# Optimization experiments

Measured on AMD Instinct MI355X. Metric: run time of the kernel, lower is better.

Reference implementation:

```python
import jax, jax.numpy as jnp
import numpy as np

B, L, LC, C, CTX, H = 4, 2048, 512, 1024, 1024, 16
D = C // H
EPS = 1e-6
SCALE = 1.0 / np.float32(np.sqrt(D))


def _ln(x):
    # LayerNorm32, elementwise_affine applied outside when present
    mu = jnp.mean(x, axis=-1, keepdims=True)
    var = jnp.var(x, axis=-1, keepdims=True)
    return (x - mu) * jax.lax.rsqrt(var + EPS)


def _attn(q, k, v):
    # q: [B,Lq,H,D], k/v: [B,Lk,H,D] -> [B,Lq,C]
    s = jnp.einsum('bqhd,bkhd->bhqk', q, k) * SCALE
    p = jax.nn.softmax(s, axis=-1)
    o = jnp.einsum('bhqk,bkhd->bqhd', p, v)
    return o.reshape(o.shape[0], o.shape[1], C)


def setup_inputs() -> dict:
    key = jax.random.key(0)
    ks = jax.random.split(key, 12)
    s = 0.02
    w = lambda k, shape: (jax.random.normal(k, shape, jnp.float32) * s)
    z = lambda n: jnp.zeros((n,), jnp.float32)
    return {
        'x': jax.random.normal(ks[0], (B, L, C), jnp.float32),
        'mod': jax.random.normal(ks[1], (B, C), jnp.float32),
        'context': jax.random.normal(ks[2], (B, LC, CTX), jnp.float32),
        'w_ada': w(ks[3], (C, 6 * C)), 'b_ada': z(6 * C),
        'w_qkv': w(ks[4], (C, 3 * C)), 'b_qkv': z(3 * C),
        'w_so': w(ks[5], (C, C)), 'b_so': z(C),
        'g_n2': jnp.ones((C,), jnp.float32), 'b_n2': z(C),
        'w_cq': w(ks[6], (C, C)), 'b_cq': z(C),
        'w_ckv': w(ks[7], (CTX, 2 * C)), 'b_ckv': z(2 * C),
        'w_co': w(ks[8], (C, C)), 'b_co': z(C),
        'w_m1': w(ks[9], (C, 4 * C)), 'b_m1': z(4 * C),
        'w_m2': w(ks[10], (4 * C, C)), 'b_m2': z(C),
    }


def reference(x, mod, context, w_ada, b_ada, w_qkv, b_qkv, w_so, b_so,
              g_n2, b_n2, w_cq, b_cq, w_ckv, b_ckv, w_co, b_co,
              w_m1, b_m1, w_m2, b_m2):
    # adaLN modulation: SiLU -> Linear(C, 6C) -> chunk(6)
    ada = jax.nn.silu(mod) @ w_ada + b_ada  # [B, 6C]
    sh_msa, sc_msa, g_msa, sh_mlp, sc_mlp, g_mlp = jnp.split(ada, 6, axis=-1)
    ex = lambda t: t[:, None, :]  # broadcast per-sample over its token run

    # --- MSA branch ---
    h = _ln(x) * (1.0 + ex(sc_msa)) + ex(sh_msa)
    qkv = (h @ w_qkv + b_qkv).reshape(B, L, 3, H, D)
    h = _attn(qkv[:, :, 0], qkv[:, :, 1], qkv[:, :, 2]) @ w_so + b_so
    x = x + h * ex(g_msa)

    # --- MCA branch (norm2 has affine) ---
    h = _ln(x) * g_n2 + b_n2
    q = (h @ w_cq + b_cq).reshape(B, L, H, D)
    kv = (context @ w_ckv + b_ckv).reshape(B, LC, 2, H, D)
    h = _attn(q, kv[:, :, 0], kv[:, :, 1]) @ w_co + b_co
    x = x + h

    # --- FFN branch ---
    h = _ln(x) * (1.0 + ex(sc_mlp)) + ex(sh_mlp)
    h = jax.nn.gelu(h @ w_m1 + b_m1, approximate=False) @ w_m2 + b_m2
    x = x + h * ex(g_mlp)
    return x
```

## Files before the change

### kernel.cpp

```cpp
#include <hip/hip_runtime.h>
#include <cstdint>

typedef __bf16 bf16;
typedef __bf16 bf16x8 __attribute__((ext_vector_type(8)));
typedef __bf16 bf16x4 __attribute__((ext_vector_type(4)));
typedef float  floatx4 __attribute__((ext_vector_type(4)));
typedef unsigned int uint32x4 __attribute__((ext_vector_type(4)));

#define B_  4
#define L_  2048
#define LC_ 512
#define C_  1024
#define H_  16
#define D_  64

typedef const __attribute__((address_space(1))) unsigned int* as1_u32p;
typedef __attribute__((address_space(3))) unsigned int* as3_u32p;

__device__ __forceinline__ void async16(const void* g, void* l) {
  __builtin_amdgcn_global_load_lds((as1_u32p)g, (as3_u32p)l, 16, 0, 0);
}

__device__ __forceinline__ floatx4 mfma16(bf16x8 a, bf16x8 b, floatx4 c) {
  return __builtin_amdgcn_mfma_f32_16x16x32_bf16(a, b, c, 0, 0, 0);
}

__device__ __forceinline__ bool dt_bf16(const unsigned* dt) { return dt[0] == 0x3F803F80u; }

__device__ __forceinline__ float rd(const void* p, size_t i, bool bf) {
  return bf ? (float)((const bf16*)p)[i] : ((const float*)p)[i];
}

__global__ __launch_bounds__(256) void k_cvt(const void* __restrict__ src, bf16* __restrict__ dst,
                                             int N, const unsigned* __restrict__ dt) {
  bool bf = dt_bf16(dt);
  int i = (blockIdx.x * 256 + threadIdx.x) * 4;
  if (i + 3 < N) {
    for (int j = 0; j < 4; ++j) dst[i + j] = (bf16)rd(src, i + j, bf);
  } else {
    for (int j = 0; j < 4 && i + j < N; ++j) dst[i + j] = (bf16)rd(src, i + j, bf);
  }
}

struct CvtSrcs { const void* s[9]; };
__global__ __launch_bounds__(256) void k_cvt_all(CvtSrcs c, bf16* __restrict__ dst,
                                                 const unsigned* __restrict__ dt) {
  bool bf = dt_bf16(dt);
  int i = blockIdx.x * 256 + threadIdx.x;
  if (i >= 15360) return;
  const int pre[10] = {0, 3072, 4096, 5120, 6144, 7168, 9216, 10240, 14336, 15360};
  int seg = 0;
  #pragma unroll
  for (int k = 1; k < 9; ++k) if (i >= pre[k]) seg = k;
  dst[i] = (bf16)rd(c.s[seg], i - pre[seg], bf);
}

__global__ __launch_bounds__(256) void k_silu(const void* __restrict__ mod, float* __restrict__ sm,
                                              const unsigned* __restrict__ dt) {
  bool bf = dt_bf16(dt);
  int i = blockIdx.x * 256 + threadIdx.x;
  if (i < B_ * C_) {
    float v = rd(mod, i, bf);
    sm[i] = v / (1.f + __expf(-v));
  }
}

__global__ __launch_bounds__(256) void k_ada(const float* __restrict__ sm, const void* __restrict__ w,
                                             float* __restrict__ part, const unsigned* __restrict__ dt) {
  bool bf = dt_bf16(dt);
  int idx = blockIdx.x * 256 + threadIdx.x;
  int b = idx / 6144, j = idx - b * 6144;
  int k0 = blockIdx.y * 256;
  const float* s = sm + b * C_;
  float acc = 0.f;
  if (bf) {
    const bf16* W = (const bf16*)w;
    for (int k = k0; k < k0 + 256; ++k) acc += s[k] * (float)W[(size_t)k * 6144 + j];
  } else {
    const float* W = (const float*)w;
    for (int k = k0; k < k0 + 256; ++k) acc += s[k] * W[(size_t)k * 6144 + j];
  }
  part[(size_t)blockIdx.y * 24576 + idx] = acc;
}

__global__ __launch_bounds__(256) void k_ada_red(const float* __restrict__ part, const void* __restrict__ bv,
                                                 float* __restrict__ ada, const unsigned* __restrict__ dt) {
  bool bf = dt_bf16(dt);
  int idx = blockIdx.x * 256 + threadIdx.x;
  int j = idx % 6144;
  ada[idx] = rd(bv, j, bf) + part[idx] + part[24576 + idx] + part[49152 + idx] + part[73728 + idx];
}

struct TransDesc { const void* src; bf16* dst; int R, Cc, nCb, pre; };
struct TransDescs { TransDesc d[7]; };
__global__ __launch_bounds__(256) void k_trans_all(TransDescs t, const unsigned* __restrict__ dt) {
  bool bf = dt_bf16(dt);
  __shared__ bf16 tile[32][33];
  int blk = blockIdx.x;
  int di = 0;
  #pragma unroll
  for (int i = 1; i < 7; ++i) if (blk >= t.d[i].pre) di = i;
  const void* src = t.d[di].src;
  bf16* dst = t.d[di].dst;
  int R = t.d[di].R, Cc = t.d[di].Cc;
  int local = blk - t.d[di].pre;
  int bx = local % t.d[di].nCb, by = local / t.d[di].nCb;
  int c0 = bx * 32, r0 = by * 32;
  int tx = threadIdx.x & 31, ty = threadIdx.x >> 5;
  for (int i = 0; i < 4; ++i)
    tile[ty * 4 + i][tx] = (bf16)rd(src, (size_t)(r0 + ty * 4 + i) * Cc + c0 + tx, bf);
  __syncthreads();
  for (int i = 0; i < 4; ++i)
    dst[(size_t)(c0 + ty * 4 + i) * R + r0 + tx] = tile[tx][ty * 4 + i];
}

__global__ __launch_bounds__(256) void k_vt(const bf16* __restrict__ src, int ld, int off, int Lk,
                                            bf16* __restrict__ VT) {
  __shared__ bf16 tile[32][33];
  int l0 = blockIdx.x * 32;
  int d0 = blockIdx.y * 32;
  int bh = blockIdx.z, b = bh >> 4, h = bh & 15;
  int tx = threadIdx.x & 31, ty = threadIdx.x >> 5;
  for (int i = 0; i < 4; ++i) {
    int l = l0 + ty * 4 + i;
    tile[ty * 4 + i][tx] = src[((size_t)b * Lk + l) * ld + off + h * 64 + d0 + tx];
  }
  __syncthreads();
  for (int i = 0; i < 4; ++i) {
    int d = d0 + ty * 4 + i;
    VT[((size_t)bh * 64 + d) * Lk + l0 + tx] = tile[tx][ty * 4 + i];
  }
}

__global__ __launch_bounds__(256) void k_ln(const void* __restrict__ xraw, const float* __restrict__ xf,
                                            const unsigned* __restrict__ dt, bf16* __restrict__ out,
                                            const float* __restrict__ ada, int scOff, int shOff, float scAdd,
                                            const bf16* __restrict__ gcol, const bf16* __restrict__ bcol) {
  int row = blockIdx.x;
  int b = row >> 11;
  int base = row * C_ + threadIdx.x * 4;
  float v[4];
  if (xf) {
    for (int i = 0; i < 4; ++i) v[i] = xf[base + i];
  } else {
    bool bf = dt_bf16(dt);
    for (int i = 0; i < 4; ++i) v[i] = rd(xraw, base + i, bf);
  }
  float s1 = 0.f, s2 = 0.f;
  for (int i = 0; i < 4; ++i) { s1 += v[i]; s2 += v[i] * v[i]; }
  for (int m = 1; m < 64; m <<= 1) { s1 += __shfl_xor(s1, m); s2 += __shfl_xor(s2, m); }
  __shared__ float r1[4], r2[4];
  int w = threadIdx.x >> 6;
  if ((threadIdx.x & 63) == 0) { r1[w] = s1; r2[w] = s2; }
  __syncthreads();
  s1 = r1[0] + r1[1] + r1[2] + r1[3];
  s2 = r2[0] + r2[1] + r2[2] + r2[3];
  float mu = s1 * (1.f / (float)C_);
  float var = fmaxf(s2 * (1.f / (float)C_) - mu * mu, 0.f);
  float rstd = rsqrtf(var + 1e-6f);
  for (int i = 0; i < 4; ++i) {
    int c = threadIdx.x * 4 + i;
    float sc, sh;
    if (ada) { sc = scAdd + ada[b * 6144 + scOff + c]; sh = ada[b * 6144 + shOff + c]; }
    else     { sc = (float)gcol[c];                    sh = (float)bcol[c]; }
    out[base + i] = (bf16)((v[i] - mu) * rstd * sc + sh);
  }
}

template <int MODE>
__global__ __launch_bounds__(256) void k_gemm(const bf16* __restrict__ A, const bf16* __restrict__ Bt,
                                              const bf16* __restrict__ bias, void* __restrict__ outv,
                                              int M, int N, int K,
                                              const void* __restrict__ resid,
                                              const float* __restrict__ ada, int gateOff,
                                              const unsigned* __restrict__ dt,
                                              float qs, int qN) {
  __shared__ bf16 As[2 * 128 * 32];
  __shared__ bf16 Bs[2 * 128 * 32];
  const int tid = threadIdx.x;
  const int w = tid >> 6, lane = tid & 63;
  const int wr = w & 1, wc = w >> 1;
  const int g = lane >> 4, t = lane & 15;

  const int nbx = gridDim.x;
  const int nwg = nbx * gridDim.y;
  const int orig = blockIdx.y * nbx + blockIdx.x;
  const int qq = nwg >> 3, rrm = nwg & 7;
  const int xcd = orig & 7, sidx = orig >> 3;
  const int wgid = (xcd < rrm ? xcd * (qq + 1) : rrm * (qq + 1) + (xcd - rrm) * qq) + sidx;
  const int rowA0 = (wgid / nbx) * 128, rowB0 = (wgid % nbx) * 128;

  const bf16* Ag = A  + (size_t)(rowA0 + w * 32 + (lane >> 2)) * K + (lane & 3) * 8;
  const bf16* Bg = Bt + (size_t)(rowB0 + w * 32 + (lane >> 2)) * K + (lane & 3) * 8;
  bf16* As0 = As + w * 1024;
  bf16* Bs0 = Bs + w * 1024;

  floatx4 acc[4][4];
  for (int i = 0; i < 4; ++i) for (int j = 0; j < 4; ++j) for (int r = 0; r < 4; ++r) acc[i][j][r] = 0.f;

  for (int kb = 0; kb < K; kb += 64) {
    async16(Ag + kb,                      As0);
    async16(Ag + kb + (size_t)16 * K,     As0 + 512);
    async16(Ag + kb + 32,                 As0 + 4096);
    async16(Ag + kb + 32 + (size_t)16 * K, As0 + 4096 + 512);
    async16(Bg + kb,                      Bs0);
    async16(Bg + kb + (size_t)16 * K,     Bs0 + 512);
    async16(Bg + kb + 32,                 Bs0 + 4096);
    async16(Bg + kb + 32 + (size_t)16 * K, Bs0 + 4096 + 512);
    __syncthreads();
    #pragma unroll
    for (int kk = 0; kk < 2; ++kk) {
      bf16x8 af[4], bfr[4];
      #pragma unroll
      for (int mt = 0; mt < 4; ++mt) af[mt]  = *(const bf16x8*)&As[kk * 4096 + (wr * 64 + mt * 16 + t) * 32 + g * 8];
      #pragma unroll
      for (int nt = 0; nt < 4; ++nt) bfr[nt] = *(const bf16x8*)&Bs[kk * 4096 + (wc * 64 + nt * 16 + t) * 32 + g * 8];
      #pragma unroll
      for (int mt = 0; mt < 4; ++mt)
        #pragma unroll
        for (int nt = 0; nt < 4; ++nt)
          acc[mt][nt] = mfma16(af[mt], bfr[nt], acc[mt][nt]);
    }
    __syncthreads();
  }

  const bool bf = (MODE == 1 || MODE == 4) ? dt_bf16(dt) : false;
  for (int mt = 0; mt < 4; ++mt) {
    for (int nt = 0; nt < 4; ++nt) {
      int grow = rowA0 + wr * 64 + mt * 16 + g * 4;
      int gcol = rowB0 + wc * 64 + nt * 16 + t;
      float bvv = (float)bias[gcol];
      for (int r = 0; r < 4; ++r) {
        int rr = grow + r;
        float v = acc[mt][nt][r] + bvv;
        size_t idx = (size_t)rr * N + gcol;
        if (MODE == 0) {
          ((bf16*)outv)[idx] = (bf16)(v * ((gcol < qN) ? qs : 1.0f));
        } else if (MODE == 1) {
          float gt = ada[(rr >> 11) * 6144 + gateOff + gcol];
          ((float*)outv)[idx] = rd(resid, idx, bf) + v * gt;
        } else if (MODE == 2) {
          ((float*)outv)[idx] = ((const float*)resid)[idx] + v;
        } else if (MODE == 3) {
          ((bf16*)outv)[idx] = (bf16)(0.5f * v * (1.f + erff(v * 0.70710678118654752f)));
        } else {
          float gt = ada[(rr >> 11) * 6144 + gateOff + gcol];
          float val = ((const float*)resid)[idx] + v * gt;
          if (bf) ((bf16*)outv)[idx] = (bf16)val;
          else    ((float*)outv)[idx] = val;
        }
      }
    }
  }
}

__global__ __launch_bounds__(256) void k_attn(const bf16* __restrict__ Qb, int ldq, int qoff,
                                              const bf16* __restrict__ Kb, int ldk, int koff,
                                              const bf16* __restrict__ VT,
                                              bf16* __restrict__ Ob, int Lk) {
  __shared__ bf16 smem[20480];

  const int tid = threadIdx.x;
  const int w = tid >> 6, lane = tid & 63;
  const int g = lane >> 4, t = lane & 15;
  const int bh = blockIdx.y, b = bh >> 4, h = bh & 15;
  const int q0 = blockIdx.x * 64;

  const bf16* Q  = Qb + (size_t)(b * L_ + q0) * ldq + h * 64 + qoff;
  const bf16* K  = Kb + (size_t)b * Lk * ldk + h * 64 + koff;
  const bf16* Vt = VT + (size_t)bh * 64 * Lk;
  bf16* O = Ob + ((size_t)(b * L_ + q0 + w * 16 + t)) * C_ + h * 64;

  const int sr0 = w * 16 + (lane >> 3), sp = lane & 7;
  const int sr1 = sr0 + 8;
  const int sw0 = (sp ^ (sr0 & 7)) * 8;
  const int sw1 = (sp ^ (sr1 & 7)) * 8;

  bf16* Ps  = smem;
  bf16* KB0 = smem + 4096;
  bf16* VB0 = smem + 12288;

  async16(Q + (size_t)sr0 * ldq + sw0, smem + w * 1024);
  async16(Q + (size_t)sr1 * ldq + sw1, smem + w * 1024 + 512);
  async16(K + (size_t)sr0 * ldk + sw0, KB0 + w * 1024);
  async16(K + (size_t)sr1 * ldk + sw1, KB0 + w * 1024 + 512);
  async16(Vt + (size_t)sr0 * Lk + sw0, VB0 + w * 1024);
  async16(Vt + (size_t)sr1 * Lk + sw1, VB0 + w * 1024 + 512);
  __syncthreads();

  const int rowQ = w * 16 + t;
  bf16x8 bq[2];
  #pragma unroll
  for (int ko = 0; ko < 2; ++ko)
    bq[ko] = *(const bf16x8*)&smem[rowQ * 64 + (((ko * 4 + g) ^ (rowQ & 7)) * 8)];

  const int nt = Lk >> 6;

  if (nt > 1) {
    async16(K + (size_t)(64 + sr0) * ldk + sw0, KB0 + 4096 + w * 1024);
    async16(K + (size_t)(64 + sr1) * ldk + sw1, KB0 + 4096 + w * 1024 + 512);
  }

  floatx4 s[4];
  __builtin_amdgcn_s_setprio(1);
  #pragma unroll
  for (int mt = 0; mt < 4; ++mt) {
    floatx4 sa; for (int r = 0; r < 4; ++r) sa[r] = 0.f;
    #pragma unroll
    for (int ko = 0; ko < 2; ++ko) {
      int rowK = mt * 16 + t;
      bf16x8 ak = *(const bf16x8*)&KB0[rowK * 64 + (((ko * 4 + g) ^ (rowK & 7)) * 8)];
      sa = mfma16(ak, bq[ko], sa);
    }
    s[mt] = sa;
  }
  __builtin_amdgcn_s_setprio(0);
  __syncthreads();

  bf16x8 ones;
  #pragma unroll
  for (int i = 0; i < 8; ++i) ones[i] = (bf16)1.0f;

  floatx4 o_acc[4], o_sum;
  for (int d = 0; d < 4; ++d) for (int r = 0; r < 4; ++r) o_acc[d][r] = 0.f;
  for (int r = 0; r < 4; ++r) o_sum[r] = 0.f;

  for (int ti = 0; ti < nt; ++ti) {
    const int cur = ti & 1;

    if (ti + 2 < nt) {
      int nx = (ti + 2) << 6;
      bf16* Kn = KB0 + cur * 4096 + w * 1024;
      async16(K + (size_t)(nx + sr0) * ldk + sw0, Kn);
      async16(K + (size_t)(nx + sr1) * ldk + sw1, Kn + 512);
    }
    if (ti + 1 < nt) {
      int nx = (ti + 1) << 6;
      bf16* Vn = VB0 + ((ti + 1) & 1) * 4096 + w * 1024;
      async16(Vt + (size_t)sr0 * Lk + nx + sw0, Vn);
      async16(Vt + (size_t)sr1 * Lk + nx + sw1, Vn + 512);
    }

    float sv[16];
    #pragma unroll
    for (int mt = 0; mt < 4; ++mt)
      #pragma unroll
      for (int r = 0; r < 4; ++r) sv[mt * 4 + r] = exp2f(s[mt][r]);

    #pragma unroll
    for (int mt = 0; mt < 4; ++mt) {
      bf16x4 pk;
      for (int r = 0; r < 4; ++r) pk[r] = (bf16)sv[mt * 4 + r];
      int off = mt * 16 + g * 4;
      int chunk = off >> 3, sub = off & 7;
      *(bf16x4*)&Ps[rowQ * 64 + ((chunk ^ (rowQ & 7)) * 8) + sub] = pk;
    }

    if (ti + 1 < nt) {
      const bf16* Kc = KB0 + ((ti + 1) & 1) * 4096;
      __builtin_amdgcn_s_setprio(1);
      #pragma unroll
      for (int mt = 0; mt < 4; ++mt) {
        floatx4 sa; for (int r = 0; r < 4; ++r) sa[r] = 0.f;
        #pragma unroll
        for (int ko = 0; ko < 2; ++ko) {
          int rowK = mt * 16 + t;
          bf16x8 ak = *(const bf16x8*)&Kc[rowK * 64 + (((ko * 4 + g) ^ (rowK & 7)) * 8)];
          sa = mfma16(ak, bq[ko], sa);
        }
        s[mt] = sa;
      }
      __builtin_amdgcn_s_setprio(0);
    }

    const bf16* Vc = VB0 + cur * 4096;
    __builtin_amdgcn_s_setprio(1);
    #pragma unroll
    for (int ko = 0; ko < 2; ++ko) {
      bf16x8 bp = *(const bf16x8*)&Ps[rowQ * 64 + (((ko * 4 + g) ^ (rowQ & 7)) * 8)];
      o_sum = mfma16(ones, bp, o_sum);
      #pragma unroll
      for (int d = 0; d < 4; ++d) {
        int rowV = d * 16 + t;
        bf16x8 av = *(const bf16x8*)&Vc[rowV * 64 + (((ko * 4 + g) ^ (rowV & 7)) * 8)];
        o_acc[d] = mfma16(av, bp, o_acc[d]);
      }
    }
    __builtin_amdgcn_s_setprio(0);

    if (ti + 1 < nt) __syncthreads();
  }

  float rl = 1.f / o_sum[0];
  #pragma unroll
  for (int d = 0; d < 4; ++d) {
    bf16x4 ov;
    for (int r = 0; r < 4; ++r) ov[r] = (bf16)(o_acc[d][r] * rl);
    *(bf16x4*)&O[d * 16 + g * 4] = ov;
  }
}

extern "C" void kernel_launch(void* const* d_in, const int* in_sizes, int n_in,
                              void* d_out, int out_size, void* d_ws, size_t ws_size,
                              hipStream_t stream) {
  const void* x     = d_in[0];
  const void* mod   = d_in[1];
  const void* ctx   = d_in[2];
  const void* w_ada = d_in[3];
  const void* b_ada = d_in[4];
  const void* w_qkv = d_in[5];
  const void* b_qkv = d_in[6];
  const void* w_so  = d_in[7];
  const void* b_so  = d_in[8];
  const void* g_n2  = d_in[9];
  const void* b_n2  = d_in[10];
  const void* w_cq  = d_in[11];
  const void* b_cq  = d_in[12];
  const void* w_ckv = d_in[13];
  const void* b_ckv = d_in[14];
  const void* w_co  = d_in[15];
  const void* b_co  = d_in[16];
  const void* w_m1  = d_in[17];
  const void* b_m1  = d_in[18];
  const void* w_m2  = d_in[19];
  const void* b_m2  = d_in[20];
  const unsigned* dt = (const unsigned*)g_n2;

  char* p = (char*)d_ws;
  auto alloc = [&](size_t bytes) { char* r = p; p += (bytes + 255) & ~(size_t)255; return r; };
  float* sm    = (float*)alloc((size_t)B_ * C_ * 4);
  float* adp   = (float*)alloc((size_t)4 * 24576 * 4);
  float* ada   = (float*)alloc((size_t)B_ * 6144 * 4);
  bf16* wT_qkv = (bf16*)alloc((size_t)3072 * 1024 * 2);
  bf16* wT_so  = (bf16*)alloc((size_t)1024 * 1024 * 2);
  bf16* wT_cq  = (bf16*)alloc((size_t)1024 * 1024 * 2);
  bf16* wT_ckv = (bf16*)alloc((size_t)2048 * 1024 * 2);
  bf16* wT_co  = (bf16*)alloc((size_t)1024 * 1024 * 2);
  bf16* wT_m1  = (bf16*)alloc((size_t)4096 * 1024 * 2);
  bf16* wT_m2  = (bf16*)alloc((size_t)1024 * 4096 * 2);
  bf16* hb     = (bf16*)alloc((size_t)8192 * 1024 * 2);
  bf16* qkvb   = (bf16*)alloc((size_t)8192 * 3072 * 2);
  bf16* attn_o = (bf16*)alloc((size_t)8192 * 1024 * 2);
  float* xcur  = (float*)alloc((size_t)8192 * 1024 * 4);
  bf16* ctxb   = (bf16*)alloc((size_t)B_ * LC_ * 1024 * 2);
  bf16* biasb  = (bf16*)alloc(15360 * 2);
  bf16* bqkvb = biasb;
  bf16* bsob  = biasb + 3072;
  bf16* g2b   = biasb + 4096;
  bf16* b2b   = biasb + 5120;
  bf16* bcqb  = biasb + 6144;
  bf16* bckvb = biasb + 7168;
  bf16* bcob  = biasb + 9216;
  bf16* bm1b  = biasb + 10240;
  bf16* bm2b  = biasb + 14336;
  bf16* q2   = qkvb;
  bf16* kv   = qkvb + (size_t)8192 * 1024;
  bf16* gbuf = qkvb;
  bf16* vt   = hb;
  if (ws_size < (size_t)(p - (char*)d_ws)) return;

  dim3 blk(256);
  k_silu<<<16, blk, 0, stream>>>(mod, sm, dt);
  k_ada<<<dim3(96, 4), blk, 0, stream>>>(sm, w_ada, adp, dt);
  k_ada_red<<<96, blk, 0, stream>>>(adp, b_ada, ada, dt);
  k_cvt<<<2048, blk, 0, stream>>>(ctx, ctxb, B_ * LC_ * 1024, dt);
  CvtSrcs cs = {{b_qkv, b_so, g_n2, b_n2, b_cq, b_ckv, b_co, b_m1, b_m2}};
  k_cvt_all<<<60, blk, 0, stream>>>(cs, biasb, dt);
  TransDescs td = {{
    {w_qkv, wT_qkv, 1024, 3072,  96, 0},
    {w_so,  wT_so,  1024, 1024,  32, 3072},
    {w_cq,  wT_cq,  1024, 1024,  32, 4096},
    {w_ckv, wT_ckv, 1024, 2048,  64, 5120},
    {w_co,  wT_co,  1024, 1024,  32, 7168},
    {w_m1,  wT_m1,  1024, 4096, 128, 8192},
    {w_m2,  wT_m2,  4096, 1024,  32, 12288},
  }};
  k_trans_all<<<16384, blk, 0, stream>>>(td, dt);

  const float SC_L2E = 0.125f * 1.44269504088896f;

  k_ln<<<8192, blk, 0, stream>>>(x, nullptr, dt, hb, ada, 1024, 0, 1.0f, nullptr, nullptr);
  k_gemm<0><<<dim3(24, 64), blk, 0, stream>>>(hb, wT_qkv, bqkvb, qkvb, 8192, 3072, 1024, nullptr, nullptr, 0, dt, SC_L2E, 1024);
  k_vt<<<dim3(64, 2, 64), blk, 0, stream>>>(qkvb, 3072, 2048, L_, vt);
  k_attn<<<dim3(32, 64), blk, 0, stream>>>(qkvb, 3072, 0, qkvb, 3072, 1024, vt, attn_o, L_);
  k_gemm<1><<<dim3(8, 64), blk, 0, stream>>>(attn_o, wT_so, bsob, xcur, 8192, 1024, 1024, x, ada, 2048, dt, 1.f, 0);

  k_ln<<<8192, blk, 0, stream>>>(nullptr, xcur, dt, hb, nullptr, 0, 0, 0.f, g2b, b2b);
  k_gemm<0><<<dim3(8, 64), blk, 0, stream>>>(hb, wT_cq, bcqb, q2, 8192, 1024, 1024, nullptr, nullptr, 0, dt, SC_L2E, 1024);
  k_gemm<0><<<dim3(16, 16), blk, 0, stream>>>(ctxb, wT_ckv, bckvb, kv, 2048, 2048, 1024, nullptr, nullptr, 0, dt, 1.f, 0);
  k_vt<<<dim3(16, 2, 64), blk, 0, stream>>>(kv, 2048, 1024, LC_, vt);
  k_attn<<<dim3(32, 64), blk, 0, stream>>>(q2, 1024, 0, kv, 2048, 0, vt, attn_o, LC_);
  k_gemm<2><<<dim3(8, 64), blk, 0, stream>>>(attn_o, wT_co, bcob, xcur, 8192, 1024, 1024, xcur, nullptr, 0, dt, 1.f, 0);

  k_ln<<<8192, blk, 0, stream>>>(nullptr, xcur, dt, hb, ada, 4096, 3072, 1.0f, nullptr, nullptr);
  k_gemm<3><<<dim3(32, 64), blk, 0, stream>>>(hb, wT_m1, bm1b, gbuf, 8192, 4096, 1024, nullptr, nullptr, 0, dt, 1.f, 0);
  k_gemm<4><<<dim3(8, 64), blk, 0, stream>>>(gbuf, wT_m2, bm2b, d_out, 8192, 1024, 4096, xcur, ada, 5120, dt, 1.f, 0);
}
```

Baseline: 835.6 us.

## Double-buffer GEMM LDS tiles and strength-reduce attention K/V prefetch addressing

```diff
diff --git a/kernel.cpp b/kernel.cpp
--- a/kernel.cpp
+++ b/kernel.cpp
@@ -175,8 +175,8 @@
                                               const float* __restrict__ ada, int gateOff,
                                               const unsigned* __restrict__ dt,
                                               float qs, int qN) {
-  __shared__ bf16 As[2 * 128 * 32];
-  __shared__ bf16 Bs[2 * 128 * 32];
+  __shared__ bf16 As[2 * 8192];
+  __shared__ bf16 Bs[2 * 8192];
   const int tid = threadIdx.x;
   const int w = tid >> 6, lane = tid & 63;
   const int wr = w & 1, wc = w >> 1;
@@ -192,36 +192,48 @@
 
   const bf16* Ag = A  + (size_t)(rowA0 + w * 32 + (lane >> 2)) * K + (lane & 3) * 8;
   const bf16* Bg = Bt + (size_t)(rowB0 + w * 32 + (lane >> 2)) * K + (lane & 3) * 8;
-  bf16* As0 = As + w * 1024;
-  bf16* Bs0 = Bs + w * 1024;
+
+  auto stage = [&](int kb, int bufsel) {
+    bf16* Ad = As + bufsel * 8192 + w * 1024;
+    bf16* Bd = Bs + bufsel * 8192 + w * 1024;
+    async16(Ag + kb,                       Ad);
+    async16(Ag + kb + (size_t)16 * K,      Ad + 512);
+    async16(Ag + kb + 32,                  Ad + 4096);
+    async16(Ag + kb + 32 + (size_t)16 * K, Ad + 4096 + 512);
+    async16(Bg + kb,                       Bd);
+    async16(Bg + kb + (size_t)16 * K,      Bd + 512);
+    async16(Bg + kb + 32,                  Bd + 4096);
+    async16(Bg + kb + 32 + (size_t)16 * K, Bd + 4096 + 512);
+  };
 
   floatx4 acc[4][4];
   for (int i = 0; i < 4; ++i) for (int j = 0; j < 4; ++j) for (int r = 0; r < 4; ++r) acc[i][j][r] = 0.f;
 
-  for (int kb = 0; kb < K; kb += 64) {
-    async16(Ag + kb,                      As0);
-    async16(Ag + kb + (size_t)16 * K,     As0 + 512);
-    async16(Ag + kb + 32,                 As0 + 4096);
-    async16(Ag + kb + 32 + (size_t)16 * K, As0 + 4096 + 512);
-    async16(Bg + kb,                      Bs0);
-    async16(Bg + kb + (size_t)16 * K,     Bs0 + 512);
-    async16(Bg + kb + 32,                 Bs0 + 4096);
-    async16(Bg + kb + 32 + (size_t)16 * K, Bs0 + 4096 + 512);
-    __syncthreads();
+  stage(0, 0);
+  __syncthreads();
+
+  const int nkb = K >> 6;
+  for (int it = 0; it < nkb; ++it) {
+    const int cur = it & 1;
+    if (it + 1 < nkb) stage((it + 1) << 6, cur ^ 1);
+    const bf16* Asb = As + cur * 8192;
+    const bf16* Bsb = Bs + cur * 8192;
+    __builtin_amdgcn_s_setprio(1);
     #pragma unroll
     for (int kk = 0; kk < 2; ++kk) {
       bf16x8 af[4], bfr[4];
       #pragma unroll
-      for (int mt = 0; mt < 4; ++mt) af[mt]  = *(const bf16x8*)&As[kk * 4096 + (wr * 64 + mt * 16 + t) * 32 + g * 8];
+      for (int mt = 0; mt < 4; ++mt) af[mt]  = *(const bf16x8*)&Asb[kk * 4096 + (wr * 64 + mt * 16 + t) * 32 + g * 8];
       #pragma unroll
-      for (int nt = 0; nt < 4; ++nt) bfr[nt] = *(const bf16x8*)&Bs[kk * 4096 + (wc * 64 + nt * 16 + t) * 32 + g * 8];
+      for (int nt = 0; nt < 4; ++nt) bfr[nt] = *(const bf16x8*)&Bsb[kk * 4096 + (wc * 64 + nt * 16 + t) * 32 + g * 8];
       #pragma unroll
       for (int mt = 0; mt < 4; ++mt)
         #pragma unroll
         for (int nt = 0; nt < 4; ++nt)
           acc[mt][nt] = mfma16(af[mt], bfr[nt], acc[mt][nt]);
     }
-    __syncthreads();
+    __builtin_amdgcn_s_setprio(0);
+    if (it + 1 < nkb) __syncthreads();
   }
 
   const bool bf = (MODE == 1 || MODE == 4) ? dt_bf16(dt) : false;
@@ -325,21 +337,26 @@
   for (int d = 0; d < 4; ++d) for (int r = 0; r < 4; ++r) o_acc[d][r] = 0.f;
   for (int r = 0; r < 4; ++r) o_sum[r] = 0.f;
 
+  const size_t kstep = (size_t)64 * ldk;
+  const bf16* Kst0 = K + (size_t)(128 + sr0) * ldk + sw0;
+  const bf16* Kst1 = K + (size_t)(128 + sr1) * ldk + sw1;
+  const bf16* Vst0 = Vt + (size_t)sr0 * Lk + 64 + sw0;
+  const bf16* Vst1 = Vt + (size_t)sr1 * Lk + 64 + sw1;
+
   for (int ti = 0; ti < nt; ++ti) {
     const int cur = ti & 1;
 
     if (ti + 2 < nt) {
-      int nx = (ti + 2) << 6;
       bf16* Kn = KB0 + cur * 4096 + w * 1024;
-      async16(K + (size_t)(nx + sr0) * ldk + sw0, Kn);
-      async16(K + (size_t)(nx + sr1) * ldk + sw1, Kn + 512);
+      async16(Kst0, Kn);
+      async16(Kst1, Kn + 512);
     }
     if (ti + 1 < nt) {
-      int nx = (ti + 1) << 6;
       bf16* Vn = VB0 + ((ti + 1) & 1) * 4096 + w * 1024;
-      async16(Vt + (size_t)sr0 * Lk + nx + sw0, Vn);
-      async16(Vt + (size_t)sr1 * Lk + nx + sw1, Vn + 512);
-    }
+      async16(Vst0, Vn);
+      async16(Vst1, Vn + 512);
+    }
+    Kst0 += kstep; Kst1 += kstep; Vst0 += 64; Vst1 += 64;
 
     float sv[16];
     #pragma unroll
```

Result: no change. 825.5 us (-1.2%).
